# Optimization experiments

Hardware: AMD Instinct MI355X
Metric: run time of the kernel (lower is better)

The kernel has to match this reference:

```python
import jax, jax.numpy as jnp
import numpy as np

DF = 2  # downsampling_factor

def _conv1x1(x, w, b):
    # x: [N,C,T,H,W], w: [O,C], b: [O]
    return jnp.einsum('ncthw,oc->nothw', x, w) + b[None, :, None, None, None]

def _avgpool(x):
    # AvgPool3d(kernel=(1,k,k), stride=(1,s,s), pad=(0,p,p)), count_include_pad=True
    k, s = DF + 1, DF
    p = (DF + 1) // 2
    summed = jax.lax.reduce_window(
        x, 0.0, jax.lax.add,
        window_dimensions=(1, 1, 1, k, k),
        window_strides=(1, 1, 1, s, s),
        padding=((0, 0), (0, 0), (0, 0), (p, p), (p, p)))
    return summed / float(k * k)

def _grid(T, Hd, Wd, t_scale):
    xg = jnp.arange(Wd, dtype=jnp.float32) / ((Wd - 1) * 0.25) - 2.0
    yg = jnp.arange(Hd, dtype=jnp.float32) / ((Hd - 1) * 0.5) - 1.0
    tg = (jnp.arange(T, dtype=jnp.float32) / ((T - 1) * 0.5) - 1.0) * t_scale
    return jnp.stack(jnp.meshgrid(tg, yg, xg, indexing='ij'), axis=0)  # [3,T,Hd,Wd]

def setup_inputs() -> dict:
    key = jax.random.key(0)
    ks = jax.random.split(key, 9)
    C, IC, OC = 256, 128, 256
    x = jax.random.normal(ks[0], (2, C, 4, 64, 64), dtype=jnp.float32)
    sc = 0.05
    return {
        'x': x,
        'theta_w': jax.random.normal(ks[1], (IC, C), jnp.float32) * sc,
        'theta_b': jax.random.normal(ks[2], (IC,), jnp.float32) * sc,
        'phi_w': jax.random.normal(ks[3], (IC, C), jnp.float32) * sc,
        'phi_b': jax.random.normal(ks[4], (IC,), jnp.float32) * sc,
        'g_w': jax.random.normal(ks[5], (IC, C), jnp.float32) * sc,
        'g_b': jax.random.normal(ks[6], (IC,), jnp.float32) * sc,
        'W_w': jax.random.normal(ks[7], (OC, IC + 3), jnp.float32) * sc,
        'W_b': jax.random.normal(ks[8], (OC,), jnp.float32) * sc,
    }

def reference(x, theta_w, theta_b, phi_w, phi_b, g_w, g_b, W_w, W_b):
    N, C, T, H, W = x.shape
    IC = theta_w.shape[0]
    theta_x = _conv1x1(x, theta_w, theta_b)                       # [N,IC,T,H,W]
    theta_x = theta_x.transpose(0, 2, 3, 4, 1).reshape(N, T * H * W, IC)
    phi_x = _avgpool(_conv1x1(x, phi_w, phi_b))                   # [N,IC,T,Hd,Wd]
    Hd, Wd = phi_x.shape[-2], phi_x.shape[-1]
    phi_x = phi_x.reshape(N, IC, T * Hd * Wd)
    f_x = jax.nn.softmax(jnp.matmul(theta_x, phi_x), axis=-1)     # [N,THW,THdWd]
    g_x = _avgpool(_conv1x1(x, g_w, g_b))                         # [N,IC,T,Hd,Wd]
    grid = _grid(T, Hd, Wd, 0.1)                                   # [3,T,Hd,Wd]
    g_x = jnp.concatenate(
        [g_x, jnp.broadcast_to(grid[None], (N, 3, T, Hd, Wd))], axis=1)
    g_x = g_x.transpose(0, 2, 3, 4, 1).reshape(N, T * Hd * Wd, IC + 3)
    y = jnp.matmul(f_x, g_x)                                       # [N,THW,IC+3]
    y = y.transpose(0, 2, 1).reshape(N, IC + 3, T, H, W)
    return _conv1x1(y, W_w, W_b)
```

## Files before the change

kernel.cpp:

```cpp
#include <hip/hip_runtime.h>
#include <stdint.h>

typedef short short8 __attribute__((ext_vector_type(8)));
typedef float floatx4 __attribute__((ext_vector_type(4)));
typedef float floatx16 __attribute__((ext_vector_type(16)));
typedef unsigned uint4v __attribute__((ext_vector_type(4)));

#define MFMA16(a, b, c) __builtin_amdgcn_mfma_f32_16x16x32_bf16((a), (b), (c), 0, 0, 0)
#define MFMA32(a, b, c) __builtin_amdgcn_mfma_f32_32x32x16_bf16((a), (b), (c), 0, 0, 0)

#define SPLITS 3
#define CHUNK_BYTES 40960
#define CHUNK_SHORTS 20480
#define VOFF_SHORTS 8704

typedef __attribute__((address_space(1))) const void* gas1_cp;
typedef __attribute__((address_space(3))) void* las3_p;

__device__ __forceinline__ void gload_lds16(const void* g, void* l) {
    __builtin_amdgcn_global_load_lds((gas1_cp)g, (las3_p)l, 16, 0, 0);
}

__device__ __forceinline__ unsigned short f2bf(float f) {
    union { float f; unsigned u; } v; v.f = f;
    unsigned u = v.u;
    unsigned r = (u + 0x7FFFu + ((u >> 16) & 1u)) >> 16;
    return (unsigned short)r;
}
__device__ __forceinline__ unsigned pkfast(float lo, float hi) {
    unsigned a = __float_as_uint(lo) + 0x8000u;
    unsigned b = __float_as_uint(hi) + 0x8000u;
    return __builtin_amdgcn_perm(b, a, 0x07060302u);
}

__global__ void k_prep(const float* th, const float* ph, const float* gw, const float* Ww,
                       unsigned short* TW, unsigned short* PW, unsigned short* GW,
                       unsigned short* Wp) {
    int i = blockIdx.x * 256 + threadIdx.x;
    if (i < 32768) {
        TW[i] = f2bf(th[i]);
    } else if (i < 65536) {
        PW[i - 32768] = f2bf(ph[i - 32768]);
    } else if (i < 98304) {
        GW[i - 65536] = f2bf(gw[i - 65536]);
    } else if (i < 98304 + 256 * 160) {
        int j = i - 98304;
        int oc = j / 160, k = j - oc * 160;
        Wp[j] = (k < 131) ? f2bf(Ww[oc * 131 + k]) : (unsigned short)0;
    }
}

__global__ void k_pool(const float* __restrict__ x, float* __restrict__ xp) {
    int e = blockIdx.x * 256 + threadIdx.x;
    int wd = e & 31, hd = (e >> 5) & 31, t = (e >> 10) & 3, c = (e >> 12) & 255, n = e >> 20;
    const float* base = x + (((size_t)(n * 256 + c) * 4 + t) << 12);
    int h0 = 2 * hd - 1, w0 = 2 * wd - 1;
    float s = 0.f;
    #pragma unroll
    for (int dh = 0; dh < 3; ++dh) {
        int h = h0 + dh;
        if ((unsigned)h < 64u) {
            const float* row = base + h * 64;
            #pragma unroll
            for (int dw = 0; dw < 3; ++dw) {
                int w = w0 + dw;
                if ((unsigned)w < 64u) s += row[w];
            }
        }
    }
    xp[((size_t)(n * 256 + c) << 12) + (t << 10) + (hd << 5) + wd] = s * (1.f / 9.f);
}

__launch_bounds__(256)
__global__ void k_convq(const float* __restrict__ x, const unsigned short* __restrict__ TW,
                        const float* __restrict__ tb, unsigned short* __restrict__ Q) {
    __shared__ unsigned short Qs[4][16][132];
    int tid = threadIdx.x, wid = tid >> 6, lane = tid & 63, quad = lane >> 4, l16 = lane & 15;
    int n = blockIdx.y;
    int px0 = blockIdx.x * 64 + wid * 16;
    const float* xb = x + ((size_t)n << 22) + px0 + l16;
    floatx4 acc[8];
    #pragma unroll
    for (int i = 0; i < 8; ++i) acc[i] = (floatx4)0.f;
    for (int kc = 0; kc < 8; ++kc) {
        int cbase = kc * 32 + quad * 8;
        uint4v bu;
        #pragma unroll
        for (int j = 0; j < 4; ++j)
            bu[j] = pkfast(xb[(size_t)(cbase + 2 * j) << 14],
                           xb[(size_t)(cbase + 2 * j + 1) << 14]);
        short8 b = __builtin_bit_cast(short8, bu);
        #pragma unroll
        for (int mt = 0; mt < 8; ++mt) {
            short8 a = *(const short8*)(TW + (mt * 16 + l16) * 256 + cbase);
            acc[mt] = MFMA16(a, b, acc[mt]);
        }
    }
    #pragma unroll
    for (int mt = 0; mt < 8; ++mt) {
        int ic = mt * 16 + quad * 4;
        uint2 w;
        w.x = pkfast(acc[mt][0] + tb[ic], acc[mt][1] + tb[ic + 1]);
        w.y = pkfast(acc[mt][2] + tb[ic + 2], acc[mt][3] + tb[ic + 3]);
        *(uint2*)&Qs[wid][l16][ic] = w;
    }
    #pragma unroll
    for (int i = 0; i < 4; ++i) {
        int pxl = i * 4 + quad;
        short8 row = *(const short8*)&Qs[wid][pxl][l16 * 8];
        *(short8*)(Q + ((((size_t)n << 14) + px0 + pxl) << 7) + l16 * 8) = row;
    }
}

__launch_bounds__(256)
__global__ void k_convkv(const float* __restrict__ xp,
                         const unsigned short* __restrict__ PW, const float* __restrict__ pb,
                         const unsigned short* __restrict__ GW, const float* __restrict__ gb,
                         unsigned short* __restrict__ Stg) {
    __shared__ unsigned short Sh[8576];
    int tid = threadIdx.x, wid = tid >> 6, lane = tid & 63, quad = lane >> 4, l16 = lane & 15;
    int n = blockIdx.y;
    int chunk = blockIdx.x;
    int k0 = chunk * 64;
    int key = k0 + wid * 16 + l16;
    unsigned short* sc = Stg + (size_t)(n * 64 + chunk) * CHUNK_SHORTS;
    const float* xb = xp + ((size_t)n << 20) + key;
    floatx4 ka[8], va[8];
    #pragma unroll
    for (int i = 0; i < 8; ++i) { ka[i] = (floatx4)0.f; va[i] = (floatx4)0.f; }
    for (int kc = 0; kc < 8; ++kc) {
        int cbase = kc * 32 + quad * 8;
        uint4v bu;
        #pragma unroll
        for (int j = 0; j < 4; ++j)
            bu[j] = pkfast(xb[(size_t)(cbase + 2 * j) << 12],
                           xb[(size_t)(cbase + 2 * j + 1) << 12]);
        short8 b = __builtin_bit_cast(short8, bu);
        #pragma unroll
        for (int mt = 0; mt < 8; ++mt) {
            short8 ap = *(const short8*)(PW + (mt * 16 + l16) * 256 + cbase);
            ka[mt] = MFMA16(ap, b, ka[mt]);
            short8 ag = *(const short8*)(GW + (mt * 16 + l16) * 256 + cbase);
            va[mt] = MFMA16(ag, b, va[mt]);
        }
    }
    int hd = (key >> 5) & 31, wdd = key & 31;
    float frac = ((hd == 0) ? 2.f : 3.f) * ((wdd == 0) ? 2.f : 3.f) * (1.f / 9.f);

    unsigned short (*Ks)[132] = (unsigned short(*)[132])(Sh + wid * 2112);
    #pragma unroll
    for (int mt = 0; mt < 8; ++mt) {
        int ic = mt * 16 + quad * 4;
        uint2 w;
        w.x = pkfast(ka[mt][0] + pb[ic] * frac, ka[mt][1] + pb[ic + 1] * frac);
        w.y = pkfast(ka[mt][2] + pb[ic + 2] * frac, ka[mt][3] + pb[ic + 3] * frac);
        *(uint2*)&Ks[l16][ic] = w;
    }
    #pragma unroll
    for (int i = 0; i < 4; ++i) {
        int pxl = i * 4 + quad;
        short8 row = *(const short8*)&Ks[pxl][l16 * 8];
        *(short8*)(sc + (wid * 16 + pxl) * 136 + l16 * 8) = row;
    }

    __syncthreads();
    unsigned short (*Vs)[134] = (unsigned short(*)[134])Sh;
    #pragma unroll
    for (int mt = 0; mt < 8; ++mt) {
        int ic = mt * 16 + quad * 4;
        uint2 w;
        w.x = pkfast(va[mt][0] + gb[ic] * frac, va[mt][1] + gb[ic + 1] * frac);
        w.y = pkfast(va[mt][2] + gb[ic + 2] * frac, va[mt][3] + gb[ic + 3] * frac);
        *(uint2*)&Vs[wid * 16 + l16][ic] = w;
    }
    __syncthreads();
    #pragma unroll
    for (int it2 = 0; it2 < 4; ++it2) {
        int ic = it2 * 32 + (tid >> 3);
        int kk = (tid & 7) * 8;
        uint4v w;
        #pragma unroll
        for (int j = 0; j < 4; ++j) {
            unsigned s0 = Vs[kk + 2 * j][ic];
            unsigned s1 = Vs[kk + 2 * j + 1][ic];
            w[j] = s0 | (s1 << 16);
        }
        *(uint4v*)(sc + VOFF_SHORTS + ic * 72 + kk) = w;
    }

    #pragma unroll
    for (int it = 0; it < 8; ++it) {
        int e = it * 256 + tid;
        int row = 128 + (e >> 6);
        int kl = e & 63;
        int kk = k0 + kl;
        int t = kk >> 10, hh = (kk >> 5) & 31, ww = kk & 31;
        unsigned short v = 0;
        if (row == 128) v = f2bf(((float)t * (1.f / 1.5f) - 1.f) * 0.1f);
        else if (row == 129) v = f2bf((float)hh * (1.f / 15.5f) - 1.f);
        else if (row == 130) v = f2bf((float)ww * (1.f / 7.75f) - 2.f);
        sc[VOFF_SHORTS + row * 72 + kl] = v;
    }
}

__device__ __forceinline__ void softmax_pv(const floatx16 st, int ks,
                                           const short (*Vlds)[72], floatx16* O,
                                           float& lacc, int l32, int half) {
    unsigned u[8];
    #pragma unroll
    for (int a = 0; a < 4; ++a) {
        float p0 = exp2f(fmaf(st[4 * a + 0], 1.44269504f, -17.3123404907f));
        float p1 = exp2f(fmaf(st[4 * a + 1], 1.44269504f, -17.3123404907f));
        float p2 = exp2f(fmaf(st[4 * a + 2], 1.44269504f, -17.3123404907f));
        float p3 = exp2f(fmaf(st[4 * a + 3], 1.44269504f, -17.3123404907f));
        lacc += (p0 + p1) + (p2 + p3);
        u[2 * a] = pkfast(p0, p1);
        u[2 * a + 1] = pkfast(p2, p3);
    }
    unsigned xu[8];
    #pragma unroll
    for (int g = 0; g < 8; ++g) xu[g] = (unsigned)__shfl_xor((int)u[g], 32);
    uint4v pw0, pw1;
    pw0[0] = half ? xu[2] : u[0];
    pw0[1] = half ? xu[3] : u[1];
    pw0[2] = half ? u[2] : xu[0];
    pw0[3] = half ? u[3] : xu[1];
    pw1[0] = half ? xu[6] : u[4];
    pw1[1] = half ? xu[7] : u[5];
    pw1[2] = half ? u[6] : xu[4];
    pw1[3] = half ? u[7] : xu[5];
    short8 pf0 = __builtin_bit_cast(short8, pw0);
    short8 pf1 = __builtin_bit_cast(short8, pw1);
    #pragma unroll
    for (int vt = 0; vt < 5; ++vt) {
        short8 vf0 = *(const short8*)&Vlds[vt * 32 + l32][ks * 32 + half * 8];
        O[vt] = MFMA32(vf0, pf0, O[vt]);
        short8 vf1 = *(const short8*)&Vlds[vt * 32 + l32][ks * 32 + 16 + half * 8];
        O[vt] = MFMA32(vf1, pf1, O[vt]);
    }
}

__launch_bounds__(256, 3)
__global__ void k_attn(const unsigned short* __restrict__ Q,
                       const unsigned char* __restrict__ Stg,
                       unsigned short* __restrict__ Y, float* __restrict__ L) {
    __shared__ __align__(16) char Sh[CHUNK_BYTES];
    int tid = threadIdx.x, wid = tid >> 6, lane = tid & 63;
    int l32 = lane & 31, half = lane >> 5;
    int n = blockIdx.y, sp = blockIdx.z;
    int c0 = (sp * 64) / SPLITS, c1 = ((sp + 1) * 64) / SPLITS;
    int nch = c1 - c0;
    int q0 = blockIdx.x * 128 + wid * 32;

    const unsigned short* Qr = Q + ((((size_t)n << 14) + q0 + l32) << 7);
    short8 qf[8];
    #pragma unroll
    for (int kc = 0; kc < 8; ++kc) qf[kc] = *(const short8*)(Qr + kc * 16 + half * 8);

    floatx16 O[5];
    #pragma unroll
    for (int t = 0; t < 5; ++t) O[t] = (floatx16)0.f;
    float lacc = 0.f;

    const short (*Klds)[136] = (const short(*)[136])Sh;
    const short (*Vlds)[72] = (const short(*)[72])(Sh + 17408);

    const unsigned char* gsl = Stg + ((size_t)(n * 64 + c0)) * CHUNK_BYTES
                               + (wid * 10) * 1024 + lane * 16;
    char* lsl = Sh + (wid * 10) * 1024;

    for (int it = 0; it < nch; ++it) {
        __syncthreads();
        const unsigned char* g = gsl + (size_t)it * CHUNK_BYTES;
        #pragma unroll
        for (int i = 0; i < 10; ++i)
            gload_lds16(g + i * 1024, lsl + i * 1024);
        asm volatile("s_waitcnt vmcnt(0)" ::: "memory");
        __syncthreads();

        #pragma unroll
        for (int ks = 0; ks < 2; ++ks) {
            floatx16 st = (floatx16)0.f;
            #pragma unroll
            for (int kc = 0; kc < 8; ++kc) {
                short8 kf = *(const short8*)&Klds[ks * 32 + l32][kc * 16 + half * 8];
                st = MFMA32(kf, qf[kc], st);
            }
            softmax_pv(st, ks, Vlds, O, lacc, l32, half);
        }
    }
    float lt = lacc + __shfl_xor(lacc, 32);
    int slab = sp * 2 + n;
    unsigned short* Yb = Y + ((((size_t)slab << 14) + q0 + l32) * 160);
    #pragma unroll
    for (int vt = 0; vt < 5; ++vt)
        #pragma unroll
        for (int g = 0; g < 4; ++g) {
            int vd = vt * 32 + 8 * g + 4 * half;
            uint2 w;
            w.x = pkfast(O[vt][4 * g], O[vt][4 * g + 1]);
            w.y = pkfast(O[vt][4 * g + 2], O[vt][4 * g + 3]);
            *(uint2*)(Yb + vd) = w;
        }
    if (lane < 32) L[(((size_t)slab) << 14) + q0 + lane] = lt;
}

__launch_bounds__(256)
__global__ void k_convf(const unsigned short* __restrict__ Y, const float* __restrict__ L,
                        const unsigned short* __restrict__ Wp, const float* __restrict__ Wb,
                        float* __restrict__ out) {
    int tid = threadIdx.x, wid = tid >> 6, lane = tid & 63, quad = lane >> 4, l16 = lane & 15;
    int n = blockIdx.y;
    int p0 = blockIdx.x * 64;
    floatx4 acc[4][4];
    #pragma unroll
    for (int i = 0; i < 4; ++i)
        #pragma unroll
        for (int j = 0; j < 4; ++j) acc[i][j] = (floatx4)0.f;
    for (int kc = 0; kc < 5; ++kc) {
        int cb = kc * 32 + quad * 8;
        short8 a[4];
        #pragma unroll
        for (int mt = 0; mt < 4; ++mt)
            a[mt] = *(const short8*)(Wp + (size_t)(wid * 64 + mt * 16 + l16) * 160 + cb);
        #pragma unroll
        for (int sp = 0; sp < SPLITS; ++sp) {
            const unsigned short* Yb = Y + ((((size_t)(sp * 2 + n)) << 14) + p0) * 160;
            #pragma unroll
            for (int nt = 0; nt < 4; ++nt) {
                short8 b = *(const short8*)(Yb + (size_t)(nt * 16 + l16) * 160 + cb);
                #pragma unroll
                for (int mt = 0; mt < 4; ++mt) acc[mt][nt] = MFMA16(a[mt], b, acc[mt][nt]);
            }
        }
    }
    float linv[4];
    #pragma unroll
    for (int nt = 0; nt < 4; ++nt) {
        int p = p0 + nt * 16 + l16;
        float ls = 0.f;
        #pragma unroll
        for (int sp = 0; sp < SPLITS; ++sp) ls += L[(((size_t)(sp * 2 + n)) << 14) + p];
        linv[nt] = 1.f / ls;
    }
    #pragma unroll
    for (int mt = 0; mt < 4; ++mt)
        #pragma unroll
        for (int r = 0; r < 4; ++r) {
            int oc = wid * 64 + mt * 16 + quad * 4 + r;
            float bb = Wb[oc];
            float* orow = out + ((((size_t)n << 8) + oc) << 14) + p0;
            #pragma unroll
            for (int nt = 0; nt < 4; ++nt)
                orow[nt * 16 + l16] = acc[mt][nt][r] * linv[nt] + bb;
        }
}

extern "C" void kernel_launch(void* const* d_in, const int* in_sizes, int n_in,
                              void* d_out, int out_size, void* d_ws, size_t ws_size,
                              hipStream_t stream) {
    (void)in_sizes; (void)n_in; (void)out_size; (void)ws_size;
    const float* x   = (const float*)d_in[0];
    const float* thw = (const float*)d_in[1];
    const float* thb = (const float*)d_in[2];
    const float* phw = (const float*)d_in[3];
    const float* phb = (const float*)d_in[4];
    const float* gw_ = (const float*)d_in[5];
    const float* gb_ = (const float*)d_in[6];
    const float* Ww  = (const float*)d_in[7];
    const float* Wb  = (const float*)d_in[8];
    float* out = (float*)d_out;

    char* ws = (char*)d_ws;
    size_t off = 0;
    auto alloc = [&](size_t b) { size_t o = off; off += (b + 255) & ~(size_t)255; return o; };
    unsigned short* TW = (unsigned short*)(ws + alloc(32768 * 2));
    unsigned short* PW = (unsigned short*)(ws + alloc(32768 * 2));
    unsigned short* GW = (unsigned short*)(ws + alloc(32768 * 2));
    unsigned short* Wp = (unsigned short*)(ws + alloc(40960 * 2));
    unsigned short* Qb = (unsigned short*)(ws + alloc((size_t)32768 * 128 * 2));
    unsigned short* St = (unsigned short*)(ws + alloc((size_t)2 * 64 * CHUNK_BYTES));
    float*          Lb = (float*)(ws + alloc((size_t)SPLITS * 2 * 16384 * 4));
    size_t ybytes = (size_t)SPLITS * 2 * 16384 * 160 * 2;
    unsigned short* Yb = (unsigned short*)(ws + alloc(ybytes));
    float*          xp = (float*)((char*)Yb + (ybytes - (size_t)2 * 256 * 4096 * 4));

    k_prep<<<(139264 + 255) / 256, 256, 0, stream>>>(thw, phw, gw_, Ww, TW, PW, GW, Wp);
    k_pool<<<8192, 256, 0, stream>>>(x, xp);
    k_convq<<<dim3(256, 2), 256, 0, stream>>>(x, TW, thb, Qb);
    k_convkv<<<dim3(64, 2), 256, 0, stream>>>(xp, PW, phb, GW, gb_, St);
    k_attn<<<dim3(128, 2, SPLITS), 256, 0, stream>>>(Qb, (const unsigned char*)St, Yb, Lb);
    k_convf<<<dim3(256, 2), 256, 0, stream>>>(Yb, Lb, Wp, Wb, out);
}
```

Measured before the change: 274.6 us.

## Pre-transpose inputs to channel-last bf16 and split K/V conv work across waves

Adds a transpose kernel that turns x into a pixel-major bf16 layout, and changes the pooling kernel to write channel-last bf16. The Q and K/V 1x1 convs can then read contiguous 16-byte channel vectors instead of strided scalar fp32 loads. The K/V conv now uses twice as many blocks over 32-key halves, with each wave doing either phi or g rather than both, to raise parallelism. The cost is an extra kernel launch and an extra round trip of x through global memory.

```diff
diff --git a/kernel.cpp b/kernel.cpp
--- a/kernel.cpp
+++ b/kernel.cpp
@@ -26,6 +26,9 @@
     unsigned u = v.u;
     unsigned r = (u + 0x7FFFu + ((u >> 16) & 1u)) >> 16;
     return (unsigned short)r;
+}
+__device__ __forceinline__ unsigned short us(float f) {
+    return (unsigned short)((__float_as_uint(f) + 0x8000u) >> 16);
 }
 __device__ __forceinline__ unsigned pkfast(float lo, float hi) {
     unsigned a = __float_as_uint(lo) + 0x8000u;
@@ -50,46 +53,82 @@
     }
 }
 
-__global__ void k_pool(const float* __restrict__ x, float* __restrict__ xp) {
-    int e = blockIdx.x * 256 + threadIdx.x;
-    int wd = e & 31, hd = (e >> 5) & 31, t = (e >> 10) & 3, c = (e >> 12) & 255, n = e >> 20;
-    const float* base = x + (((size_t)(n * 256 + c) * 4 + t) << 12);
+__launch_bounds__(256)
+__global__ void k_xt(const float* __restrict__ x, unsigned short* __restrict__ xT) {
+    __shared__ unsigned short Xs[64][40];
+    int tid = threadIdx.x;
+    int n = blockIdx.y;
+    int px0 = (blockIdx.x & 255) * 64;
+    int c0 = (blockIdx.x >> 8) * 32;
+    #pragma unroll
+    for (int p = 0; p < 2; ++p) {
+        int c = c0 + p * 16 + (tid >> 4);
+        int l = tid & 15;
+        const float* src = x + (((size_t)(n * 256 + c)) << 14) + px0 + 4 * l;
+        float4 v = *(const float4*)src;
+        int cc = c - c0;
+        Xs[4 * l + 0][cc] = us(v.x);
+        Xs[4 * l + 1][cc] = us(v.y);
+        Xs[4 * l + 2][cc] = us(v.z);
+        Xs[4 * l + 3][cc] = us(v.w);
+    }
+    __syncthreads();
+    int px = tid >> 2, c8 = (tid & 3) * 8;
+    short8 row = *(const short8*)&Xs[px][c8];
+    *(short8*)(xT + (((size_t)n << 14) + px0 + px) * 256 + c0 + c8) = row;
+}
+
+__launch_bounds__(256)
+__global__ void k_poolT(const float* __restrict__ x, unsigned short* __restrict__ xpT) {
+    __shared__ unsigned short P[32][40];
+    int tid = threadIdx.x;
+    int n = blockIdx.y;
+    int r = blockIdx.x & 127;
+    int c0 = (blockIdx.x >> 7) * 32;
+    int t = r >> 5, hd = r & 31;
+    int wd = tid & 31;
+    int cg = (tid >> 5) * 4;
     int h0 = 2 * hd - 1, w0 = 2 * wd - 1;
-    float s = 0.f;
-    #pragma unroll
-    for (int dh = 0; dh < 3; ++dh) {
-        int h = h0 + dh;
-        if ((unsigned)h < 64u) {
-            const float* row = base + h * 64;
-            #pragma unroll
-            for (int dw = 0; dw < 3; ++dw) {
-                int w = w0 + dw;
-                if ((unsigned)w < 64u) s += row[w];
+    #pragma unroll
+    for (int jj = 0; jj < 4; ++jj) {
+        int c = c0 + cg + jj;
+        const float* base = x + (((size_t)(n * 256 + c) * 4 + t) << 12);
+        float s = 0.f;
+        #pragma unroll
+        for (int dh = 0; dh < 3; ++dh) {
+            int h = h0 + dh;
+            if ((unsigned)h < 64u) {
+                const float* row = base + h * 64;
+                #pragma unroll
+                for (int dw = 0; dw < 3; ++dw) {
+                    int w = w0 + dw;
+                    if ((unsigned)w < 64u) s += row[w];
+                }
             }
         }
-    }
-    xp[((size_t)(n * 256 + c) << 12) + (t << 10) + (hd << 5) + wd] = s * (1.f / 9.f);
+        P[wd][cg + jj] = us(s * (1.f / 9.f));
+    }
+    __syncthreads();
+    int key = r * 32 + (tid >> 3);
+    int cc = (tid & 7) * 4;
+    uint2 w = *(const uint2*)&P[tid >> 3][cc];
+    *(uint2*)(xpT + (((size_t)n << 12) + key) * 256 + c0 + cc) = w;
 }
 
 __launch_bounds__(256)
-__global__ void k_convq(const float* __restrict__ x, const unsigned short* __restrict__ TW,
+__global__ void k_convq(const unsigned short* __restrict__ xT, const unsigned short* __restrict__ TW,
                         const float* __restrict__ tb, unsigned short* __restrict__ Q) {
     __shared__ unsigned short Qs[4][16][132];
     int tid = threadIdx.x, wid = tid >> 6, lane = tid & 63, quad = lane >> 4, l16 = lane & 15;
     int n = blockIdx.y;
     int px0 = blockIdx.x * 64 + wid * 16;
-    const float* xb = x + ((size_t)n << 22) + px0 + l16;
+    const unsigned short* xb = xT + (((size_t)n << 14) + px0 + l16) * 256;
     floatx4 acc[8];
     #pragma unroll
     for (int i = 0; i < 8; ++i) acc[i] = (floatx4)0.f;
     for (int kc = 0; kc < 8; ++kc) {
         int cbase = kc * 32 + quad * 8;
-        uint4v bu;
-        #pragma unroll
-        for (int j = 0; j < 4; ++j)
-            bu[j] = pkfast(xb[(size_t)(cbase + 2 * j) << 14],
-                           xb[(size_t)(cbase + 2 * j + 1) << 14]);
-        short8 b = __builtin_bit_cast(short8, bu);
+        short8 b = *(const short8*)(xb + cbase);
         #pragma unroll
         for (int mt = 0; mt < 8; ++mt) {
             short8 a = *(const short8*)(TW + (mt * 16 + l16) * 256 + cbase);
@@ -113,71 +152,68 @@
 }
 
 __launch_bounds__(256)
-__global__ void k_convkv(const float* __restrict__ xp,
+__global__ void k_convkv(const unsigned short* __restrict__ xpT,
                          const unsigned short* __restrict__ PW, const float* __restrict__ pb,
                          const unsigned short* __restrict__ GW, const float* __restrict__ gb,
                          unsigned short* __restrict__ Stg) {
-    __shared__ unsigned short Sh[8576];
+    __shared__ unsigned short Ks[2][16][132];
+    __shared__ unsigned short Vs[32][132];
     int tid = threadIdx.x, wid = tid >> 6, lane = tid & 63, quad = lane >> 4, l16 = lane & 15;
     int n = blockIdx.y;
-    int chunk = blockIdx.x;
-    int k0 = chunk * 64;
-    int key = k0 + wid * 16 + l16;
+    int c32 = blockIdx.x;
+    int chunk = c32 >> 1, half = c32 & 1;
+    int k0 = c32 * 32;
+    int role = wid >> 1, kg = wid & 1;
+    int key = k0 + kg * 16 + l16;
     unsigned short* sc = Stg + (size_t)(n * 64 + chunk) * CHUNK_SHORTS;
-    const float* xb = xp + ((size_t)n << 20) + key;
-    floatx4 ka[8], va[8];
-    #pragma unroll
-    for (int i = 0; i < 8; ++i) { ka[i] = (floatx4)0.f; va[i] = (floatx4)0.f; }
+    const unsigned short* xb = xpT + (((size_t)n << 12) + key) * 256;
+    const unsigned short* W = role ? GW : PW;
+    const float* bias = role ? gb : pb;
+    floatx4 acc[8];
+    #pragma unroll
+    for (int i = 0; i < 8; ++i) acc[i] = (floatx4)0.f;
     for (int kc = 0; kc < 8; ++kc) {
         int cbase = kc * 32 + quad * 8;
-        uint4v bu;
-        #pragma unroll
-        for (int j = 0; j < 4; ++j)
-            bu[j] = pkfast(xb[(size_t)(cbase + 2 * j) << 12],
-                           xb[(size_t)(cbase + 2 * j + 1) << 12]);
-        short8 b = __builtin_bit_cast(short8, bu);
+        short8 b = *(const short8*)(xb + cbase);
         #pragma unroll
         for (int mt = 0; mt < 8; ++mt) {
-            short8 ap = *(const short8*)(PW + (mt * 16 + l16) * 256 + cbase);
-            ka[mt] = MFMA16(ap, b, ka[mt]);
-            short8 ag = *(const short8*)(GW + (mt * 16 + l16) * 256 + cbase);
-            va[mt] = MFMA16(ag, b, va[mt]);
+            short8 a = *(const short8*)(W + (mt * 16 + l16) * 256 + cbase);
+            acc[mt] = MFMA16(a, b, acc[mt]);
         }
     }
     int hd = (key >> 5) & 31, wdd = key & 31;
     float frac = ((hd == 0) ? 2.f : 3.f) * ((wdd == 0) ? 2.f : 3.f) * (1.f / 9.f);
 
-    unsigned short (*Ks)[132] = (unsigned short(*)[132])(Sh + wid * 2112);
-    #pragma unroll
-    for (int mt = 0; mt < 8; ++mt) {
-        int ic = mt * 16 + quad * 4;
-        uint2 w;
-        w.x = pkfast(ka[mt][0] + pb[ic] * frac, ka[mt][1] + pb[ic + 1] * frac);
-        w.y = pkfast(ka[mt][2] + pb[ic + 2] * frac, ka[mt][3] + pb[ic + 3] * frac);
-        *(uint2*)&Ks[l16][ic] = w;
-    }
-    #pragma unroll
-    for (int i = 0; i < 4; ++i) {
-        int pxl = i * 4 + quad;
-        short8 row = *(const short8*)&Ks[pxl][l16 * 8];
-        *(short8*)(sc + (wid * 16 + pxl) * 136 + l16 * 8) = row;
-    }
-
+    if (role == 0) {
+        #pragma unroll
+        for (int mt = 0; mt < 8; ++mt) {
+            int ic = mt * 16 + quad * 4;
+            uint2 w;
+            w.x = pkfast(acc[mt][0] + bias[ic] * frac, acc[mt][1] + bias[ic + 1] * frac);
+            w.y = pkfast(acc[mt][2] + bias[ic + 2] * frac, acc[mt][3] + bias[ic + 3] * frac);
+            *(uint2*)&Ks[kg][l16][ic] = w;
+        }
+        #pragma unroll
+        for (int i = 0; i < 4; ++i) {
+            int pxl = i * 4 + quad;
+            short8 row = *(const short8*)&Ks[kg][pxl][l16 * 8];
+            *(short8*)(sc + (half * 32 + kg * 16 + pxl) * 136 + l16 * 8) = row;
+        }
+    } else {
+        #pragma unroll
+        for (int mt = 0; mt < 8; ++mt) {
+            int ic = mt * 16 + quad * 4;
+            uint2 w;
+            w.x = pkfast(acc[mt][0] + bias[ic] * frac, acc[mt][1] + bias[ic + 1] * frac);
+            w.y = pkfast(acc[mt][2] + bias[ic + 2] * frac, acc[mt][3] + bias[ic + 3] * frac);
+            *(uint2*)&Vs[kg * 16 + l16][ic] = w;
+        }
+    }
     __syncthreads();
-    unsigned short (*Vs)[134] = (unsigned short(*)[134])Sh;
-    #pragma unroll
-    for (int mt = 0; mt < 8; ++mt) {
-        int ic = mt * 16 + quad * 4;
-        uint2 w;
-        w.x = pkfast(va[mt][0] + gb[ic] * frac, va[mt][1] + gb[ic + 1] * frac);
-        w.y = pkfast(va[mt][2] + gb[ic + 2] * frac, va[mt][3] + gb[ic + 3] * frac);
-        *(uint2*)&Vs[wid * 16 + l16][ic] = w;
-    }
-    __syncthreads();
-    #pragma unroll
-    for (int it2 = 0; it2 < 4; ++it2) {
-        int ic = it2 * 32 + (tid >> 3);
-        int kk = (tid & 7) * 8;
+    #pragma unroll
+    for (int it2 = 0; it2 < 2; ++it2) {
+        int ic = it2 * 64 + (tid >> 2);
+        int kk = (tid & 3) * 8;
         uint4v w;
         #pragma unroll
         for (int j = 0; j < 4; ++j) {
@@ -185,21 +221,20 @@
             unsigned s1 = Vs[kk + 2 * j + 1][ic];
             w[j] = s0 | (s1 << 16);
         }
-        *(uint4v*)(sc + VOFF_SHORTS + ic * 72 + kk) = w;
-    }
-
-    #pragma unroll
-    for (int it = 0; it < 8; ++it) {
+        *(uint4v*)(sc + VOFF_SHORTS + ic * 72 + half * 32 + kk) = w;
+    }
+    #pragma unroll
+    for (int it = 0; it < 4; ++it) {
         int e = it * 256 + tid;
-        int row = 128 + (e >> 6);
-        int kl = e & 63;
+        int row = 128 + (e >> 5);
+        int kl = e & 31;
         int kk = k0 + kl;
         int t = kk >> 10, hh = (kk >> 5) & 31, ww = kk & 31;
         unsigned short v = 0;
         if (row == 128) v = f2bf(((float)t * (1.f / 1.5f) - 1.f) * 0.1f);
         else if (row == 129) v = f2bf((float)hh * (1.f / 15.5f) - 1.f);
         else if (row == 130) v = f2bf((float)ww * (1.f / 7.75f) - 2.f);
-        sc[VOFF_SHORTS + row * 72 + kl] = v;
+        sc[VOFF_SHORTS + row * 72 + half * 32 + kl] = v;
     }
 }
 
@@ -382,13 +417,15 @@
     unsigned short* St = (unsigned short*)(ws + alloc((size_t)2 * 64 * CHUNK_BYTES));
     float*          Lb = (float*)(ws + alloc((size_t)SPLITS * 2 * 16384 * 4));
     size_t ybytes = (size_t)SPLITS * 2 * 16384 * 160 * 2;
-    unsigned short* Yb = (unsigned short*)(ws + alloc(ybytes));
-    float*          xp = (float*)((char*)Yb + (ybytes - (size_t)2 * 256 * 4096 * 4));
+    unsigned short* Yb  = (unsigned short*)(ws + alloc(ybytes));
+    unsigned short* xT  = Yb;
+    unsigned short* xpT = (unsigned short*)((char*)Yb + (size_t)2 * 16384 * 256 * 2);
 
     k_prep<<<(139264 + 255) / 256, 256, 0, stream>>>(thw, phw, gw_, Ww, TW, PW, GW, Wp);
-    k_pool<<<8192, 256, 0, stream>>>(x, xp);
-    k_convq<<<dim3(256, 2), 256, 0, stream>>>(x, TW, thb, Qb);
-    k_convkv<<<dim3(64, 2), 256, 0, stream>>>(xp, PW, phb, GW, gb_, St);
+    k_xt<<<dim3(2048, 2), 256, 0, stream>>>(x, xT);
+    k_poolT<<<dim3(1024, 2), 256, 0, stream>>>(x, xpT);
+    k_convq<<<dim3(256, 2), 256, 0, stream>>>(xT, TW, thb, Qb);
+    k_convkv<<<dim3(128, 2), 256, 0, stream>>>(xpT, PW, phb, GW, gb_, St);
     k_attn<<<dim3(128, 2, SPLITS), 256, 0, stream>>>(Qb, (const unsigned char*)St, Yb, Lb);
     k_convf<<<dim3(256, 2), 256, 0, stream>>>(Yb, Lb, Wp, Wb, out);
 }
```

Measured after the change: 255.2 us. 1.08x faster.
